# Kernel optimization log

Hardware: AMD Instinct MI355X
Metric: run time of the kernel (lower is better)

The kernel has to match this reference:

```python
import jax, jax.numpy as jnp
import numpy as np

B, S, D = 8, 1024, 1024
H, DK = 16, 64  # num_heads, d_k; H*DK == D
NEG_INF = 1e29


def setup_inputs() -> dict:
    key = jax.random.key(0)
    ks = jax.random.split(key, 12)
    sc = 1.0 / np.sqrt(D)
    q = jax.random.normal(ks[0], (B, S, D), jnp.float32)
    k = jax.random.normal(ks[1], (B, S, D), jnp.float32)
    v = jax.random.normal(ks[2], (B, S, D), jnp.float32)
    # causal mask, broadcast per batch (mask==0 positions are masked out)
    mask = jnp.broadcast_to(jnp.tril(jnp.ones((S, S), jnp.int32)), (B, S, S))
    Wq = jax.random.normal(ks[3], (D, D), jnp.float32) * sc
    bq = jax.random.normal(ks[4], (D,), jnp.float32) * 0.01
    Wk = jax.random.normal(ks[5], (D, D), jnp.float32) * sc
    bk = jax.random.normal(ks[6], (D,), jnp.float32) * 0.01
    Wv = jax.random.normal(ks[7], (D, D), jnp.float32) * sc
    bv = jax.random.normal(ks[8], (D,), jnp.float32) * 0.01
    Wo = jax.random.normal(ks[9], (D, D), jnp.float32) * sc
    bo = jax.random.normal(ks[10], (D,), jnp.float32) * 0.01
    return {"q": q, "k": k, "v": v, "mask": mask,
            "Wq": Wq, "bq": bq, "Wk": Wk, "bk": bk,
            "Wv": Wv, "bv": bv, "Wo": Wo, "bo": bo}


def reference(q, k, v, mask, Wq, bq, Wk, bk, Wv, bv, Wo, bo):
    # Linear projections (torch Linear: x @ W.T + b)
    q1 = q @ Wq.T + bq
    k1 = k @ Wk.T + bk
    v1 = v @ Wv.T + bv
    # [B, S, D] -> [B, H, S, DK]
    def split_heads(x):
        return x.reshape(B, S, H, DK).transpose(0, 2, 1, 3)
    q3, k3, v3 = split_heads(q1), split_heads(k1), split_heads(v1)
    # scores [B, H, S, S]
    scores = jnp.einsum('bhqd,bhkd->bhqk', q3, k3) / jnp.sqrt(jnp.float32(DK))
    scores = jnp.where(mask[:, None, :, :] == 0, -NEG_INF, scores)
    probs = jax.nn.softmax(scores, axis=-1)
    attn = jnp.einsum('bhqk,bhkd->bhqd', probs, v3)  # [B, H, S, DK]
    out = attn.transpose(0, 2, 1, 3).reshape(B, S, D)
    return out @ Wo.T + bo
```

## Files before the change

### kernel.cpp

```cpp
#include <hip/hip_runtime.h>
#include <hip/hip_bf16.h>
#include <stdint.h>

constexpr int NB = 8;
constexpr int NS = 1024;
constexpr int ND = 1024;
constexpr int NH = 16;
constexpr int NDK = 64;
constexpr int NT = NS / 64;
constexpr int NKT = ND / 64;

typedef __bf16 bf16_t;
typedef __attribute__((ext_vector_type(8))) __bf16 bf16x8;
typedef __attribute__((ext_vector_type(4))) __bf16 bf16x4;
typedef __attribute__((ext_vector_type(4))) float f32x4;

#define GLL16(g, s) __builtin_amdgcn_global_load_lds( \
    (const __attribute__((address_space(1))) void*)(g), \
    (__attribute__((address_space(3))) void*)(s), 16, 0, 0)

__device__ __forceinline__ void cvt_body(const float* __restrict__ s,
                                         bf16_t* __restrict__ d, long n) {
  long i0 = (long)(blockIdx.x * blockDim.x + threadIdx.x) * 4;
  long step = (long)gridDim.x * blockDim.x * 4;
  for (long i = i0; i < n; i += step) {
    float4 f = *(const float4*)(s + i);
    bf16x4 o;
    o[0] = (bf16_t)f.x; o[1] = (bf16_t)f.y; o[2] = (bf16_t)f.z; o[3] = (bf16_t)f.w;
    *(bf16x4*)(d + i) = o;
  }
}

__global__ __launch_bounds__(256) void cvt4_kernel(const float* s0, bf16_t* d0,
                                                   const float* s1, bf16_t* d1,
                                                   const float* s2, bf16_t* d2,
                                                   const float* s3, bf16_t* d3, long n) {
  const float* s = blockIdx.y == 0 ? s0 : blockIdx.y == 1 ? s1 : blockIdx.y == 2 ? s2 : s3;
  bf16_t* d = blockIdx.y == 0 ? d0 : blockIdx.y == 1 ? d1 : blockIdx.y == 2 ? d2 : d3;
  cvt_body(s, d, n);
}

__global__ __launch_bounds__(512, 2) void gemm_qkv(
    const float* A0, const bf16_t* W0, const float* b0, bf16_t* C0,
    const float* A1, const bf16_t* W1, const float* b1, bf16_t* C1,
    const float* A2, const bf16_t* W2, const float* b2, bf16_t* C2) {
  __shared__ bf16_t S[2 * 16384 + 3 * 8192];
  const int o = blockIdx.x;
  const int xcd = o & 7, s = o >> 3;
  const int bx = s & 7, u = s >> 3;
  const int zby = xcd + 8 * u;
  const int z = zby >> 5, by = zby & 31;
  const float* A = z == 0 ? A0 : z == 1 ? A1 : A2;
  const bf16_t* W = z == 0 ? W0 : z == 1 ? W1 : W2;
  const float* bb = z == 0 ? b0 : z == 1 ? b1 : b2;
  bf16_t* C = z == 0 ? C0 : z == 1 ? C1 : C2;

  const int tid = threadIdx.x;
  const int l = tid & 63, w = tid >> 6;
  const int wr = w >> 1, wc = w & 1;
  const int g = l >> 4, r = l & 15;
  const int m0 = by * 256, n0 = bx * 128;
  const int wbase = w * 512;

  bf16_t* Ab = S;
  bf16_t* Bb = S + 32768;

  float4 faA[8], faB[8];
  auto issueA = [&](int t, float4 (&dst)[8]) {
#pragma unroll
    for (int it = 0; it < 4; ++it) {
      const float* p = A + (size_t)(m0 + it * 64 + (tid >> 3)) * ND + t * 64 + (tid & 7) * 8;
      dst[it * 2]     = *(const float4*)p;
      dst[it * 2 + 1] = *(const float4*)(p + 4);
    }
  };
  auto writeA = [&](int ab, float4 (&src)[8]) {
#pragma unroll
    for (int it = 0; it < 4; ++it) {
      int row = it * 64 + (tid >> 3), c = tid & 7;
      bf16x8 ov;
      ov[0] = (bf16_t)src[it * 2].x;     ov[1] = (bf16_t)src[it * 2].y;
      ov[2] = (bf16_t)src[it * 2].z;     ov[3] = (bf16_t)src[it * 2].w;
      ov[4] = (bf16_t)src[it * 2 + 1].x; ov[5] = (bf16_t)src[it * 2 + 1].y;
      ov[6] = (bf16_t)src[it * 2 + 1].z; ov[7] = (bf16_t)src[it * 2 + 1].w;
      *(bf16x8*)(Ab + ab * 16384 + row * 64 + ((c ^ (row & 7)) << 3)) = ov;
    }
  };
  auto stageB = [&](int qb, int t) {
#pragma unroll
    for (int it = 0; it < 2; ++it) {
      int idx = it * 512 + tid;
      int row = idx >> 3, c = (idx & 7) ^ (row & 7);
      GLL16(W + (size_t)(n0 + row) * ND + (t << 6) + c * 8,
            Bb + qb * 8192 + it * 4096 + wbase);
    }
  };

  f32x4 acc[4][4] = {};

  issueA(0, faA);
  issueA(1, faB);
  stageB(0, 0);
  stageB(1, 1);
  asm volatile("s_waitcnt vmcnt(2)" ::: "memory");
  __builtin_amdgcn_sched_barrier(0);
  writeA(0, faA);
  asm volatile("s_waitcnt lgkmcnt(0)" ::: "memory");
  __builtin_amdgcn_s_barrier();

  auto bodyT = [&](int t, float4 (&fiss)[8], float4 (&fwr)[8]) {
    if (t + 2 < NKT) issueA(t + 2, fiss);
    __builtin_amdgcn_sched_barrier(0);
    if (t + 2 < NKT) stageB((t + 2) % 3, t + 2);
    __builtin_amdgcn_sched_barrier(0);

    const bf16_t* a_ = Ab + (t & 1) * 16384;
    const bf16_t* b_ = Bb + (t % 3) * 8192;
#pragma unroll
    for (int kk = 0; kk < 2; ++kk) {
      bf16x8 af[4], bw[4];
#pragma unroll
      for (int m = 0; m < 4; ++m) {
        int row = wr * 64 + m * 16 + r;
        af[m] = *(const bf16x8*)(a_ + row * 64 + (((kk * 4 + g) ^ (row & 7)) << 3));
      }
#pragma unroll
      for (int n = 0; n < 4; ++n) {
        int row = wc * 64 + n * 16 + r;
        bw[n] = *(const bf16x8*)(b_ + row * 64 + (((kk * 4 + g) ^ (row & 7)) << 3));
      }
      __builtin_amdgcn_s_setprio(1);
#pragma unroll
      for (int m = 0; m < 4; ++m)
#pragma unroll
        for (int n = 0; n < 4; ++n)
          acc[m][n] = __builtin_amdgcn_mfma_f32_16x16x32_bf16(af[m], bw[n], acc[m][n], 0, 0, 0);
      __builtin_amdgcn_s_setprio(0);
    }

    if (t + 2 < NKT)      asm volatile("s_waitcnt vmcnt(10)" ::: "memory");
    else                  asm volatile("s_waitcnt vmcnt(0)" ::: "memory");
    __builtin_amdgcn_sched_barrier(0);
    if (t + 1 < NKT) writeA((t + 1) & 1, fwr);
    asm volatile("s_waitcnt lgkmcnt(0)" ::: "memory");
    __builtin_amdgcn_s_barrier();
  };

#pragma unroll 1
  for (int tt = 0; tt < NKT; tt += 2) {
    bodyT(tt, faA, faB);
    bodyT(tt + 1, faB, faA);
  }

  if (z == 2) {
#pragma unroll
    for (int n = 0; n < 4; ++n) {
      int col = n0 + wc * 64 + n * 16 + r;
      int hh = col >> 6, dk = col & 63;
      float bv = bb[col];
#pragma unroll
      for (int m = 0; m < 4; ++m) {
        int row0 = m0 + wr * 64 + m * 16 + g * 4;
        int b_ = row0 >> 10, s0 = row0 & 1023;
        bf16x4 o4;
#pragma unroll
        for (int j = 0; j < 4; ++j) o4[j] = (bf16_t)(acc[m][n][j] + bv);
        *(bf16x4*)(C + (((size_t)b_ * 16 + hh) * 64 + dk) * 1024 + s0) = o4;
      }
    }
  } else {
#pragma unroll
    for (int n = 0; n < 4; ++n) {
      int col = n0 + wc * 64 + n * 16 + r;
      float bv = bb[col];
#pragma unroll
      for (int m = 0; m < 4; ++m) {
        int row0 = m0 + wr * 64 + m * 16 + g * 4;
#pragma unroll
        for (int j = 0; j < 4; ++j)
          C[(size_t)(row0 + j) * ND + col] = (bf16_t)(acc[m][n][j] + bv);
      }
    }
  }
}

__global__ __launch_bounds__(512, 2) void gemm_bt(const bf16_t* __restrict__ A,
                                                  const bf16_t* __restrict__ W,
                                                  const float* __restrict__ bias,
                                                  float* __restrict__ Cout,
                                                  int M, int N, int K) {
  __shared__ bf16_t S[3 * 24576];
  const int o = blockIdx.x;
  const int xcd = o & 7, s = o >> 3;
  const int bx = s & 7, u = s >> 3;
  const int by = xcd + 8 * u;

  const int tid = threadIdx.x;
  const int l = tid & 63, w = tid >> 6;
  const int wr = w >> 1, wc = w & 1;
  const int g = l >> 4, r = l & 15;
  const int m0 = by * 256, n0 = bx * 128;
  const int wbase = w * 512;

  auto stageA2 = [&](int q, int t, int half) {
#pragma unroll
    for (int it = half * 2; it < half * 2 + 2; ++it) {
      int idx = it * 512 + tid;
      int row = idx >> 3, c = (idx & 7) ^ (row & 7);
      GLL16(A + (size_t)(m0 + row) * K + (t << 6) + c * 8,
            S + q * 24576 + it * 4096 + wbase);
    }
  };
  auto stageB2 = [&](int q, int t) {
#pragma unroll
    for (int it = 0; it < 2; ++it) {
      int idx = it * 512 + tid;
      int row = idx >> 3, c = (idx & 7) ^ (row & 7);
      GLL16(W + (size_t)(n0 + row) * K + (t << 6) + c * 8,
            S + q * 24576 + 16384 + it * 4096 + wbase);
    }
  };

  f32x4 acc[4][4] = {};
  const int NKT2 = K >> 6;

  stageA2(0, 0, 0); stageA2(0, 0, 1); stageB2(0, 0);
  stageA2(1, 1, 0); stageA2(1, 1, 1); stageB2(1, 1);

  int q = 0;
  for (int t = 0; t < NKT2; ++t) {
    const bool pf = (t + 2 < NKT2);
    int q2 = q + 2; if (q2 >= 3) q2 -= 3;

    if (t + 1 < NKT2) asm volatile("s_waitcnt vmcnt(6)" ::: "memory");
    else              asm volatile("s_waitcnt vmcnt(0)" ::: "memory");
    __builtin_amdgcn_s_barrier();

    const bf16_t* a_ = S + q * 24576;
    const bf16_t* b_ = a_ + 16384;

#pragma unroll
    for (int kk = 0; kk < 2; ++kk) {
      bf16x8 bw[4];
#pragma unroll
      for (int n = 0; n < 4; ++n) {
        int row = wc * 64 + n * 16 + r;
        bw[n] = *(const bf16x8*)(b_ + row * 64 + (((kk * 4 + g) ^ (row & 7)) << 3));
      }
#pragma unroll
      for (int mh = 0; mh < 2; ++mh) {
        bf16x8 af[2];
#pragma unroll
        for (int i = 0; i < 2; ++i) {
          int row = wr * 64 + (mh * 2 + i) * 16 + r;
          af[i] = *(const bf16x8*)(a_ + row * 64 + (((kk * 4 + g) ^ (row & 7)) << 3));
        }
        if (pf) {
          int ph = kk * 2 + mh;
          if (ph == 0)      stageA2(q2, t + 2, 0);
          else if (ph == 1) stageA2(q2, t + 2, 1);
          else if (ph == 2) stageB2(q2, t + 2);
        }
        __builtin_amdgcn_s_barrier();
        asm volatile("s_waitcnt lgkmcnt(0)" ::: "memory");
        __builtin_amdgcn_sched_barrier(0);
        __builtin_amdgcn_s_setprio(1);
#pragma unroll
        for (int i = 0; i < 2; ++i)
#pragma unroll
          for (int n = 0; n < 4; ++n)
            acc[mh * 2 + i][n] = __builtin_amdgcn_mfma_f32_16x16x32_bf16(
                af[i], bw[n], acc[mh * 2 + i][n], 0, 0, 0);
        __builtin_amdgcn_s_setprio(0);
        __builtin_amdgcn_sched_barrier(0);
      }
    }
    ++q; if (q >= 3) q -= 3;
  }

#pragma unroll
  for (int n = 0; n < 4; ++n) {
    int col = n0 + wc * 64 + n * 16 + r;
    float bv = bias[col];
#pragma unroll
    for (int m = 0; m < 4; ++m) {
      int row0 = m0 + wr * 64 + m * 16 + g * 4;
#pragma unroll
      for (int j = 0; j < 4; ++j)
        Cout[(size_t)(row0 + j) * N + col] = acc[m][n][j] + bv;
    }
  }
}

__global__ __launch_bounds__(256, 4) void attn_kernel(const bf16_t* __restrict__ Q1,
                                                      const bf16_t* __restrict__ K1,
                                                      const bf16_t* __restrict__ V1t,
                                                      bf16_t* __restrict__ attn) {
  __shared__ bf16_t Kt[2][64 * 64];
  __shared__ bf16_t Vt[2][64 * 64];
  __shared__ bf16_t Pl[4][16 * 64];

  const int tid = threadIdx.x;
  const int l = tid & 63, w = tid >> 6;
  const int g = l >> 4, r = l & 15;

  const int o = blockIdx.x;
  const int os = (o & 7) * 128 + (o >> 3);
  const int pair = os & 7, hb = os >> 3;
  const int h = hb & 15, b = hb >> 4;

  constexpr float SC = 0.18033688011112042f;
  const bf16_t* vbase = V1t + ((size_t)(b * 16 + h) * 64) * 1024;

  for (int ph = 0; ph < 2; ++ph) {
    const int qt = ph ? (NT - 1 - pair) : pair;
    const int qrow_g = qt * 64 + w * 16 + r;

    const bf16_t* qptr = Q1 + ((size_t)b * NS + qrow_g) * ND + h * 64;
    bf16x8 qf0 = *(const bf16x8*)(qptr + g * 8);
    bf16x8 qf1 = *(const bf16x8*)(qptr + 32 + g * 8);
#pragma unroll
    for (int i = 0; i < 8; ++i) {
      qf0[i] = (bf16_t)((float)qf0[i] * SC);
      qf1[i] = (bf16_t)((float)qf1[i] * SC);
    }

    float mrun = -1e30f, lrun = 0.f;
    f32x4 oacc[4] = {};

    __syncthreads();

    auto stageKV = [&](int kt2, int pb) {
      const int k0 = kt2 * 64;
#pragma unroll
      for (int it = 0; it < 2; ++it) {
        int idx = it * 256 + tid;
        int row = idx >> 3;
        int c = (idx & 7) ^ (row & 7);
        GLL16(K1 + ((size_t)b * NS + k0 + row) * ND + h * 64 + c * 8,
              &Kt[pb][(it * 256 + w * 64) * 8]);
      }
#pragma unroll
      for (int it = 0; it < 2; ++it) {
        int idx = it * 256 + tid;
        int row = idx >> 3;
        int c = (idx & 7) ^ (row & 7);
        GLL16(vbase + (size_t)row * 1024 + k0 + c * 8,
              &Vt[pb][(it * 256 + w * 64) * 8]);
      }
    };

    stageKV(0, 0);

    for (int kt = 0; kt <= qt; ++kt) {
      const int p = kt & 1;
      const int k0 = kt * 64;

      __syncthreads();

      if (kt < qt) stageKV(kt + 1, p ^ 1);

      f32x4 sacc[4] = {};
      __builtin_amdgcn_s_setprio(1);
#pragma unroll
      for (int n = 0; n < 4; ++n) {
        int key = n * 16 + r;
#pragma unroll
        for (int kk = 0; kk < 2; ++kk) {
          int dk2 = kk * 32 + g * 8;
          int boff = key * 128 + ((dk2 * 2) ^ ((key & 7) << 4));
          bf16x8 kf = *(const bf16x8*)((char*)Kt[p] + boff);
          sacc[n] = __builtin_amdgcn_mfma_f32_16x16x32_bf16(kf, kk == 0 ? qf0 : qf1, sacc[n], 0, 0, 0);
        }
      }
      __builtin_amdgcn_s_setprio(0);

      if (kt == qt) {
#pragma unroll
        for (int n = 0; n < 4; ++n)
#pragma unroll
          for (int j = 0; j < 4; ++j)
            if (k0 + n * 16 + g * 4 + j > qrow_g) sacc[n][j] = -1e30f;
      }

      float mx;
      {
        float t0 = fmaxf(fmaxf(sacc[0][0], sacc[0][1]), fmaxf(sacc[0][2], sacc[0][3]));
        float t1 = fmaxf(fmaxf(sacc[1][0], sacc[1][1]), fmaxf(sacc[1][2], sacc[1][3]));
        float t2 = fmaxf(fmaxf(sacc[2][0], sacc[2][1]), fmaxf(sacc[2][2], sacc[2][3]));
        float t3 = fmaxf(fmaxf(sacc[3][0], sacc[3][1]), fmaxf(sacc[3][2], sacc[3][3]));
        mx = fmaxf(fmaxf(t0, t1), fmaxf(t2, t3));
      }
      mx = fmaxf(mx, __shfl_xor(mx, 16));
      mx = fmaxf(mx, __shfl_xor(mx, 32));

      if (!__all(mx <= mrun + 8.0f)) {
        float m_new = fmaxf(mrun, mx);
        float esc = __builtin_amdgcn_exp2f(mrun - m_new);
        mrun = m_new;
        lrun *= esc;
#pragma unroll
        for (int n = 0; n < 4; ++n)
#pragma unroll
          for (int j = 0; j < 4; ++j) oacc[n][j] *= esc;
      }

      float rsum = 0.f;
#pragma unroll
      for (int n = 0; n < 4; ++n) {
        bf16x4 p4;
#pragma unroll
        for (int j = 0; j < 4; ++j) {
          float pe = __builtin_amdgcn_exp2f(sacc[n][j] - mrun);
          rsum += pe;
          p4[j] = (bf16_t)pe;
        }
        *(bf16x4*)((char*)Pl[w] + r * 128 + ((n * 32 + g * 8) ^ ((r & 7) << 4))) = p4;
      }
      rsum += __shfl_xor(rsum, 16);
      rsum += __shfl_xor(rsum, 32);
      lrun += rsum;

      __builtin_amdgcn_s_setprio(1);
#pragma unroll
      for (int kk = 0; kk < 2; ++kk) {
        bf16x8 pf = *(const bf16x8*)((char*)Pl[w] + r * 128 + ((kk * 64 + g * 16) ^ ((r & 7) << 4)));
#pragma unroll
        for (int n = 0; n < 4; ++n) {
          int dkr = n * 16 + r;
          bf16x8 vf = *(const bf16x8*)((char*)Vt[p] + dkr * 128 + ((kk * 64 + g * 16) ^ ((dkr & 7) << 4)));
          oacc[n] = __builtin_amdgcn_mfma_f32_16x16x32_bf16(vf, pf, oacc[n], 0, 0, 0);
        }
      }
      __builtin_amdgcn_s_setprio(0);
    }

    float linv = 1.0f / lrun;
#pragma unroll
    for (int n = 0; n < 4; ++n) {
      bf16x4 o4;
#pragma unroll
      for (int j = 0; j < 4; ++j) o4[j] = (bf16_t)(oacc[n][j] * linv);
      *(bf16x4*)(attn + ((size_t)b * NS + qrow_g) * ND + h * 64 + n * 16 + g * 4) = o4;
    }
  }
}

extern "C" void kernel_launch(void* const* d_in, const int* in_sizes, int n_in,
                              void* d_out, int out_size, void* d_ws, size_t ws_size,
                              hipStream_t stream) {
  const float* q  = (const float*)d_in[0];
  const float* k  = (const float*)d_in[1];
  const float* v  = (const float*)d_in[2];
  const float* Wq = (const float*)d_in[4];
  const float* bq = (const float*)d_in[5];
  const float* Wk = (const float*)d_in[6];
  const float* bk = (const float*)d_in[7];
  const float* Wv = (const float*)d_in[8];
  const float* bv = (const float*)d_in[9];
  const float* Wo = (const float*)d_in[10];
  const float* bo = (const float*)d_in[11];
  float* out = (float*)d_out;

  const size_t NX = (size_t)NB * NS * ND;
  const size_t NW = (size_t)ND * ND;
  char* ws = (char*)d_ws;
  size_t off = 0;
  auto alloc = [&](size_t bytes) {
    char* p = ws + off;
    off += (bytes + 255) & ~(size_t)255;
    return p;
  };
  bf16_t* wqb = (bf16_t*)alloc(NW * 2);
  bf16_t* wkb = (bf16_t*)alloc(NW * 2);
  bf16_t* wvb = (bf16_t*)alloc(NW * 2);
  bf16_t* wob = (bf16_t*)alloc(NW * 2);
  bf16_t* q1  = (bf16_t*)alloc(NX * 2);
  bf16_t* k1  = (bf16_t*)alloc(NX * 2);
  bf16_t* v1t = (bf16_t*)alloc(NX * 2);
  bf16_t* at  = (bf16_t*)alloc(NX * 2);

  dim3 blk(256);
  cvt4_kernel<<<dim3(128, 4), blk, 0, stream>>>(Wq, wqb, Wk, wkb, Wv, wvb, Wo, wob, (long)NW);

  gemm_qkv<<<dim3(768), dim3(512), 0, stream>>>(
      q, wqb, bq, q1, k, wkb, bk, k1, v, wvb, bv, v1t);

  attn_kernel<<<dim3((NT / 2) * NH * NB), blk, 0, stream>>>(q1, k1, v1t, at);

  gemm_bt<<<dim3(256), dim3(512), 0, stream>>>(at, wob, bo, out, NB * NS, ND, ND);
}
```

Before: 145.3 us.

## Enlarge attention query tile to 128 rows with 8 waves per block

The attention kernel now uses 512-thread blocks, with 8 waves each handling 16 query rows, so a block covers a 128-row query tile. Each K/V tile staged in shared memory is reused across twice as many queries, which halves global K/V traffic and staging per query. Each thread issues one load per tensor instead of two. The causal mask now applies to the last two key tiles, and the grid shrinks to 512 blocks. The trade-offs are fewer blocks, more LDS per block, and wasted masked work on the diagonal tiles.

```diff
diff --git a/kernel.cpp b/kernel.cpp
--- a/kernel.cpp
+++ b/kernel.cpp
@@ -7,7 +7,6 @@
 constexpr int ND = 1024;
 constexpr int NH = 16;
 constexpr int NDK = 64;
-constexpr int NT = NS / 64;
 constexpr int NKT = ND / 64;
 
 typedef __bf16 bf16_t;
@@ -292,29 +291,39 @@
   }
 }
 
-__global__ __launch_bounds__(256, 4) void attn_kernel(const bf16_t* __restrict__ Q1,
+__global__ __launch_bounds__(512, 4) void attn_kernel(const bf16_t* __restrict__ Q1,
                                                       const bf16_t* __restrict__ K1,
                                                       const bf16_t* __restrict__ V1t,
                                                       bf16_t* __restrict__ attn) {
   __shared__ bf16_t Kt[2][64 * 64];
   __shared__ bf16_t Vt[2][64 * 64];
-  __shared__ bf16_t Pl[4][16 * 64];
+  __shared__ bf16_t Pl[8][16 * 64];
 
   const int tid = threadIdx.x;
   const int l = tid & 63, w = tid >> 6;
   const int g = l >> 4, r = l & 15;
 
   const int o = blockIdx.x;
-  const int os = (o & 7) * 128 + (o >> 3);
-  const int pair = os & 7, hb = os >> 3;
+  const int os = (o & 7) * 64 + (o >> 3);
+  const int pair = os & 3, hb = os >> 2;
   const int h = hb & 15, b = hb >> 4;
 
   constexpr float SC = 0.18033688011112042f;
   const bf16_t* vbase = V1t + ((size_t)(b * 16 + h) * 64) * 1024;
 
+  auto stageKV = [&](int kt2, int pb) {
+    const int k0 = kt2 * 64;
+    int row = tid >> 3;
+    int c = (tid & 7) ^ (row & 7);
+    GLL16(K1 + ((size_t)b * NS + k0 + row) * ND + h * 64 + c * 8,
+          &Kt[pb][w * 512]);
+    GLL16(vbase + (size_t)row * 1024 + k0 + c * 8,
+          &Vt[pb][w * 512]);
+  };
+
   for (int ph = 0; ph < 2; ++ph) {
-    const int qt = ph ? (NT - 1 - pair) : pair;
-    const int qrow_g = qt * 64 + w * 16 + r;
+    const int qt = ph ? (7 - pair) : pair;
+    const int qrow_g = qt * 128 + w * 16 + r;
 
     const bf16_t* qptr = Q1 + ((size_t)b * NS + qrow_g) * ND + h * 64;
     bf16x8 qf0 = *(const bf16x8*)(qptr + g * 8);
@@ -330,35 +339,16 @@
 
     __syncthreads();
 
-    auto stageKV = [&](int kt2, int pb) {
-      const int k0 = kt2 * 64;
-#pragma unroll
-      for (int it = 0; it < 2; ++it) {
-        int idx = it * 256 + tid;
-        int row = idx >> 3;
-        int c = (idx & 7) ^ (row & 7);
-        GLL16(K1 + ((size_t)b * NS + k0 + row) * ND + h * 64 + c * 8,
-              &Kt[pb][(it * 256 + w * 64) * 8]);
-      }
-#pragma unroll
-      for (int it = 0; it < 2; ++it) {
-        int idx = it * 256 + tid;
-        int row = idx >> 3;
-        int c = (idx & 7) ^ (row & 7);
-        GLL16(vbase + (size_t)row * 1024 + k0 + c * 8,
-              &Vt[pb][(it * 256 + w * 64) * 8]);
-      }
-    };
-
+    const int nkt = 2 * qt + 2;
     stageKV(0, 0);
 
-    for (int kt = 0; kt <= qt; ++kt) {
+    for (int kt = 0; kt < nkt; ++kt) {
       const int p = kt & 1;
       const int k0 = kt * 64;
 
       __syncthreads();
 
-      if (kt < qt) stageKV(kt + 1, p ^ 1);
+      if (kt + 1 < nkt) stageKV(kt + 1, p ^ 1);
 
       f32x4 sacc[4] = {};
       __builtin_amdgcn_s_setprio(1);
@@ -375,7 +365,7 @@
       }
       __builtin_amdgcn_s_setprio(0);
 
-      if (kt == qt) {
+      if (kt >= 2 * qt) {
 #pragma unroll
         for (int n = 0; n < 4; ++n)
 #pragma unroll
@@ -486,7 +476,7 @@
   gemm_qkv<<<dim3(768), dim3(512), 0, stream>>>(
       q, wqb, bq, q1, k, wkb, bk, k1, v, wvb, bv, v1t);
 
-  attn_kernel<<<dim3((NT / 2) * NH * NB), blk, 0, stream>>>(q1, k1, v1t, at);
+  attn_kernel<<<dim3(512), dim3(512), 0, stream>>>(q1, k1, v1t, at);
 
   gemm_bt<<<dim3(256), dim3(512), 0, stream>>>(at, wob, bo, out, NB * NS, ND, ND);
 }
```

New measurement: 144.4 us. No clear change (-0.6%).
